# Kernel optimization log

Hardware: AMD Instinct MI355X
Metric: run time of the kernel (lower is better)

## Reference

```python
import jax, jax.numpy as jnp
import numpy as np

N = 1_000_000
D = 128            # node feature dim
G = 25_000         # number of graphs (num_segments, static)
STEPS = 8


def setup_inputs() -> dict:
    key = jax.random.key(0)
    k1, k2, k3 = jax.random.split(key, 3)
    node_feature = jax.random.normal(k1, (N, D), dtype=jnp.float32)
    graph_indicator = jnp.sort(jax.random.randint(k2, (N,), 0, G, dtype=jnp.int32))
    # glorot-ish small init for recurrent kernel (carry_dim=2D -> 4*D gates)
    recurrent_kernel = jax.random.normal(k3, (2 * D, 4 * D), dtype=jnp.float32) * 0.05
    bias = jnp.zeros((4 * D,), dtype=jnp.float32)
    return {
        "node_feature": node_feature,
        "graph_indicator": graph_indicator,
        "recurrent_kernel": recurrent_kernel,
        "bias": bias,
    }


def _segment_softmax(score, seg_ids, num_segments):
    # numerically-stable per-segment softmax over a flat score vector [N]
    smax = jax.ops.segment_max(score, seg_ids, num_segments=num_segments)
    e = jnp.exp(score - smax[seg_ids])
    denom = jax.ops.segment_sum(e, seg_ids, num_segments=num_segments)
    return e / denom[seg_ids]


def reference(node_feature, graph_indicator, recurrent_kernel, bias):
    d = node_feature.shape[-1]
    memory_state = jnp.zeros((G, d), dtype=node_feature.dtype)
    carry_state = jnp.zeros((G, d), dtype=node_feature.dtype)
    carry_state_evolved = None
    for _ in range(STEPS):
        # attention score per node: <node_feature, carry of its graph>
        carry_exp = carry_state[graph_indicator]                  # [N, d]
        score = jnp.sum(node_feature * carry_exp, axis=1)         # [N]
        attn = _segment_softmax(score, graph_indicator, G)        # [N]
        readout = jax.ops.segment_sum(attn[:, None] * node_feature,
                                      graph_indicator, num_segments=G)  # [G, d]
        carry_state_evolved = jnp.concatenate([carry_state, readout], axis=1)  # [G, 2d]
        # NoInputLSTMCell
        z = carry_state_evolved @ recurrent_kernel + bias          # [G, 4d]
        u, f, c, o = jnp.split(z, 4, axis=1)
        memory_state = jax.nn.sigmoid(f) * memory_state + jax.nn.sigmoid(u) * jnp.tanh(c)
        carry_state = jax.nn.sigmoid(o) * jnp.tanh(memory_state)
    return carry_state_evolved
```

## Files before the change

kernel.cpp:

```cpp
#include <hip/hip_runtime.h>
#include <stdint.h>

#define DD   128
#define G2D  256
#define G4D  512
#define GPB  8
#define SLOT 64
#define ASTR 264

typedef float  f32x4  __attribute__((ext_vector_type(4)));
typedef short  s16x4  __attribute__((ext_vector_type(4)));
typedef short  s16x8  __attribute__((ext_vector_type(8)));
typedef __bf16 bf16x8 __attribute__((ext_vector_type(8)));

__device__ __forceinline__ short f2bf(float f) {
  unsigned u = __builtin_bit_cast(unsigned, f);
  u += 0x7FFFu + ((u >> 16) & 1u);
  return (short)(u >> 16);
}
__device__ __forceinline__ float bf2f(short s) {
  unsigned u = ((unsigned)(unsigned short)s) << 16;
  return __builtin_bit_cast(float, u);
}
__device__ __forceinline__ float sigmoidf_(float x) {
  return 1.f / (1.f + __expf(-x));
}
__device__ __forceinline__ float tanhf_(float x) {
  x = fminf(fmaxf(x, -15.f), 15.f);
  float e = __expf(2.f * x);
  return (e - 1.f) / (e + 1.f);
}

__global__ void seg_kernel(const int* __restrict__ ind, int* __restrict__ seg,
                           int N, int G) {
  int g = blockIdx.x * blockDim.x + threadIdx.x;
  if (g > G) return;
  int lo = 0, hi = N;
  while (lo < hi) {
    int mid = (lo + hi) >> 1;
    if (ind[mid] < g) lo = mid + 1; else hi = mid;
  }
  seg[g] = lo;
}

__global__ void wconv_kernel(const float* __restrict__ W, short* __restrict__ WT) {
  int idx = blockIdx.x * blockDim.x + threadIdx.x;
  int n = idx & (G4D - 1);
  int k = idx >> 9;
  WT[(size_t)n * G2D + k] = f2bf(W[(size_t)k * G4D + n]);
}

__global__ void __launch_bounds__(512) fused_kernel(
    const float* __restrict__ nf, const int* __restrict__ seg,
    const short* __restrict__ WT, const float* __restrict__ bias,
    float* __restrict__ out, int G) {
  extern __shared__ char smem[];
  short* nfb   = (short*)smem;
  short* A     = (short*)(smem + GPB * SLOT * DD * 2);
  float* carry = (float*)(smem + GPB * SLOT * DD * 2 + 16 * ASTR * 2);
  float* mem   = (float*)((char*)carry + GPB * DD * 4);

  const int t    = threadIdx.x;
  const int w    = t >> 6;
  const int lane = t & 63;
  const int gq   = lane >> 4;
  const int sl   = lane & 15;
  const int g0   = blockIdx.x * GPB;
  const int g    = g0 + w;
  const bool active = (g < G);

  {
    int* az = (int*)A;
    for (int i = t; i < (16 * ASTR) / 2; i += 512) az[i] = 0;
    for (int i = t; i < GPB * DD; i += 512) mem[i] = 0.f;
  }
  int s0 = 0, n = 0;
  if (active) { s0 = seg[g]; n = seg[g + 1] - s0; }
  carry[w * DD + lane]      = 0.f;
  carry[w * DD + 64 + lane] = 0.f;
  __syncthreads();

  short* slot = nfb + w * (SLOT * DD);
  const int nl = n < SLOT ? n : SLOT;
  {
    const int r2 = lane >> 5;
    const int c  = lane & 31;
    const int iters = (nl + 1) >> 1;
    f32x4 vc; int rowc = r2; bool okc = rowc < nl;
    if (okc) vc = *((const f32x4*)(nf + (size_t)(s0 + rowc) * DD) + c);
    for (int i = 0; i < iters; ++i) {
      const int rown = (i + 1) * 2 + r2;
      f32x4 vn; const bool okn = rown < nl;
      if (okn) vn = *((const f32x4*)(nf + (size_t)(s0 + rown) * DD) + c);
      if (okc) {
        s16x4 o;
        o[0] = f2bf(vc.x); o[1] = f2bf(vc.y); o[2] = f2bf(vc.z); o[3] = f2bf(vc.w);
        *(s16x4*)(slot + (size_t)rowc * DD + c * 4) = o;
      }
      vc = vn; rowc = rown; okc = okn;
    }
  }

  s16x8 bw[8][4];
  #pragma unroll
  for (int kc = 0; kc < 8; ++kc) {
    const int k0 = kc * 32 + gq * 8;
    #pragma unroll
    for (int gi = 0; gi < 4; ++gi) {
      const int ncol = gi * DD + w * 16 + sl;
      bw[kc][gi] = *(const s16x8*)(WT + (size_t)ncol * G2D + k0);
    }
  }
  const int colB = w * 16 + sl;
  const float bU = bias[0 * DD + colB], bF = bias[1 * DD + colB],
              bC = bias[2 * DD + colB], bO = bias[3 * DD + colB];

  #pragma unroll 1
  for (int step = 0; step < 8; ++step) {
    float r[8];
    #pragma unroll
    for (int k = 0; k < 8; ++k) r[k] = 0.f;

    if (active && n > 0) {
      float m = -1e30f, l = 0.f;
      float acc[8];
      #pragma unroll
      for (int k = 0; k < 8; ++k) acc[k] = 0.f;

      if (step == 0) {
        const int nfull = nl >> 2, rem = nl & 3;
        #pragma unroll 2
        for (int i = 0; i < nfull; ++i) {
          s16x8 xr = *(const s16x8*)(slot + (size_t)(i * 4 + gq) * DD + sl * 8);
          #pragma unroll
          for (int k = 0; k < 8; ++k) acc[k] += bf2f(xr[k]);
          l += 1.f;
        }
        if (gq < rem) {
          s16x8 xr = *(const s16x8*)(slot + (size_t)(nfull * 4 + gq) * DD + sl * 8);
          #pragma unroll
          for (int k = 0; k < 8; ++k) acc[k] += bf2f(xr[k]);
          l += 1.f;
        }
        for (int j = SLOT + gq; j < n; j += 4) {
          const f32x4* gp = (const f32x4*)(nf + (size_t)(s0 + j) * DD) + sl * 2;
          const f32x4 a = gp[0], b = gp[1];
          const float xf[8] = {a.x, a.y, a.z, a.w, b.x, b.y, b.z, b.w};
          #pragma unroll
          for (int k = 0; k < 8; ++k) acc[k] += xf[k];
          l += 1.f;
        }
        m = 0.f;
      } else {
        const f32x4 c0 = *(const f32x4*)(carry + w * DD + sl * 8);
        const f32x4 c1 = *(const f32x4*)(carry + w * DD + sl * 8 + 4);
        auto upd = [&](const float xf[8]) {
          float s = xf[0] * c0.x + xf[1] * c0.y + xf[2] * c0.z + xf[3] * c0.w
                  + xf[4] * c1.x + xf[5] * c1.y + xf[6] * c1.z + xf[7] * c1.w;
          #pragma unroll
          for (int off = 1; off < 16; off <<= 1) s += __shfl_xor(s, off, 64);
          const float nm = fmaxf(m, s);
          const float sc = __expf(m - nm);
          const float p  = __expf(s - nm);
          l = l * sc + p;
          #pragma unroll
          for (int k = 0; k < 8; ++k) acc[k] = acc[k] * sc + p * xf[k];
          m = nm;
        };
        const int nfull = nl >> 2, rem = nl & 3;
        #pragma unroll 2
        for (int i = 0; i < nfull; ++i) {
          s16x8 xr = *(const s16x8*)(slot + (size_t)(i * 4 + gq) * DD + sl * 8);
          float xf[8];
          #pragma unroll
          for (int k = 0; k < 8; ++k) xf[k] = bf2f(xr[k]);
          upd(xf);
        }
        if (gq < rem) {
          s16x8 xr = *(const s16x8*)(slot + (size_t)(nfull * 4 + gq) * DD + sl * 8);
          float xf[8];
          #pragma unroll
          for (int k = 0; k < 8; ++k) xf[k] = bf2f(xr[k]);
          upd(xf);
        }
        for (int j = SLOT + gq; j < n; j += 4) {
          const f32x4* gp = (const f32x4*)(nf + (size_t)(s0 + j) * DD) + sl * 2;
          const f32x4 a = gp[0], b = gp[1];
          const float xf[8] = {a.x, a.y, a.z, a.w, b.x, b.y, b.z, b.w};
          upd(xf);
        }
      }
      #pragma unroll
      for (int ww = 16; ww <= 32; ww <<= 1) {
        const float m2 = __shfl_xor(m, ww, 64);
        const float l2 = __shfl_xor(l, ww, 64);
        const float M  = fmaxf(m, m2);
        const float e1 = __expf(m - M);
        const float e2 = __expf(m2 - M);
        l = l * e1 + l2 * e2;
        #pragma unroll
        for (int k = 0; k < 8; ++k) {
          const float a2 = __shfl_xor(acc[k], ww, 64);
          acc[k] = acc[k] * e1 + a2 * e2;
        }
        m = M;
      }
      if (gq == 0) {
        const float inv = (l > 0.f) ? 1.f / l : 0.f;
        s16x8 pk;
        #pragma unroll
        for (int k = 0; k < 8; ++k) { r[k] = acc[k] * inv; pk[k] = f2bf(r[k]); }
        *(s16x8*)(A + w * ASTR + DD + sl * 8) = pk;
      }
    }

    if (step == 7) {
      if (active) {
        if (gq == 0) {
          f32x4 r0 = {r[0], r[1], r[2], r[3]};
          f32x4 r1 = {r[4], r[5], r[6], r[7]};
          *(f32x4*)(out + (size_t)g * G2D + DD + sl * 8)     = r0;
          *(f32x4*)(out + (size_t)g * G2D + DD + sl * 8 + 4) = r1;
        } else if (gq == 1) {
          const f32x4 a = *(const f32x4*)(carry + w * DD + sl * 8);
          const f32x4 b = *(const f32x4*)(carry + w * DD + sl * 8 + 4);
          *(f32x4*)(out + (size_t)g * G2D + sl * 8)     = a;
          *(f32x4*)(out + (size_t)g * G2D + sl * 8 + 4) = b;
        }
      }
      break;
    }
    __syncthreads();

    f32x4 az[4];
    #pragma unroll
    for (int gi = 0; gi < 4; ++gi) az[gi] = (f32x4){0.f, 0.f, 0.f, 0.f};
    #pragma unroll
    for (int kc = 0; kc < 8; ++kc) {
      const int k0 = kc * 32 + gq * 8;
      const s16x8 af = *(const s16x8*)(A + (size_t)sl * ASTR + k0);
      #pragma unroll
      for (int gi = 0; gi < 4; ++gi)
        az[gi] = __builtin_amdgcn_mfma_f32_16x16x32_bf16(
            __builtin_bit_cast(bf16x8, af), __builtin_bit_cast(bf16x8, bw[kc][gi]),
            az[gi], 0, 0, 0);
    }
    __syncthreads();
    if (gq < 2) {
      #pragma unroll
      for (int rr = 0; rr < 4; ++rr) {
        const int gg = gq * 4 + rr;
        if (g0 + gg < G) {
          const float u = az[0][rr] + bU;
          const float f = az[1][rr] + bF;
          const float c = az[2][rr] + bC;
          const float o = az[3][rr] + bO;
          const float mo = mem[gg * DD + colB];
          const float mn = sigmoidf_(f) * mo + sigmoidf_(u) * tanhf_(c);
          mem[gg * DD + colB] = mn;
          const float cn = sigmoidf_(o) * tanhf_(mn);
          carry[gg * DD + colB] = cn;
          A[gg * ASTR + colB] = f2bf(cn);
        }
      }
    }
    __syncthreads();
  }
}

extern "C" void kernel_launch(void* const* d_in, const int* in_sizes, int n_in,
                              void* d_out, int out_size, void* d_ws, size_t ws_size,
                              hipStream_t stream) {
  const float* nf   = (const float*)d_in[0];
  const int*   ind  = (const int*)d_in[1];
  const float* W    = (const float*)d_in[2];
  const float* bias = (const float*)d_in[3];
  int N = in_sizes[1];
  int G = out_size / G2D;

  char* ws = (char*)d_ws;
  short* WT  = (short*)ws;
  int*   seg = (int*)(ws + 262144);
  (void)ws_size; (void)n_in;

  seg_kernel<<<(G + 256) / 256, 256, 0, stream>>>(ind, seg, N, G);
  wconv_kernel<<<(G2D * G4D) / 256, 256, 0, stream>>>(W, WT);

  const int SMEM_BYTES = GPB * SLOT * DD * 2
                       + 16 * ASTR * 2
                       + GPB * DD * 4
                       + GPB * DD * 4;
  static bool attr_set = false;
  if (!attr_set) {
    hipFuncSetAttribute(reinterpret_cast<const void*>(fused_kernel),
                        hipFuncAttributeMaxDynamicSharedMemorySize, SMEM_BYTES);
    attr_set = true;
  }
  fused_kernel<<<(G + GPB - 1) / GPB, 512, SMEM_BYTES, stream>>>(
      nf, seg, WT, bias, (float*)d_out, G);
}
```

Baseline: 1.319 ms.

## Split each graph across two waves with DPP reductions and lazy softmax rescaling

Doubles the block to 1024 threads so each graph is processed by two wavefronts, each taking half the nodes. The two partial online-softmax states are merged through a shared buffer, and the LSTM gate matmul is split so each wave computes two of the four gate groups. The shuffle-based 16-lane score reduction is replaced with DPP row adds, and the online softmax only rescales when the max grows by more than 8. This adds extra barriers and shared-memory traffic for the merges, and halves the registers available per thread.

Result: slower. 1.411 ms (+7.0%).

```diff
diff --git a/kernel.cpp b/kernel.cpp
--- a/kernel.cpp
+++ b/kernel.cpp
@@ -11,6 +11,7 @@
 typedef float  f32x4  __attribute__((ext_vector_type(4)));
 typedef short  s16x4  __attribute__((ext_vector_type(4)));
 typedef short  s16x8  __attribute__((ext_vector_type(8)));
+typedef int    i32x4  __attribute__((ext_vector_type(4)));
 typedef __bf16 bf16x8 __attribute__((ext_vector_type(8)));
 
 __device__ __forceinline__ short f2bf(float f) {
@@ -18,9 +19,9 @@
   u += 0x7FFFu + ((u >> 16) & 1u);
   return (short)(u >> 16);
 }
-__device__ __forceinline__ float bf2f(short s) {
-  unsigned u = ((unsigned)(unsigned short)s) << 16;
-  return __builtin_bit_cast(float, u);
+__device__ __forceinline__ void unpack2(int w_, float& lo, float& hi) {
+  lo = __builtin_bit_cast(float, (int)(w_ << 16));
+  hi = __builtin_bit_cast(float, (int)(w_ & 0xFFFF0000));
 }
 __device__ __forceinline__ float sigmoidf_(float x) {
   return 1.f / (1.f + __expf(-x));
@@ -29,6 +30,20 @@
   x = fminf(fmaxf(x, -15.f), 15.f);
   float e = __expf(2.f * x);
   return (e - 1.f) / (e + 1.f);
+}
+
+template <int CTRL>
+__device__ __forceinline__ float dppadd_(float v) {
+  const int x = __builtin_amdgcn_update_dpp(
+      0, __builtin_bit_cast(int, v), CTRL, 0xF, 0xF, true);
+  return v + __builtin_bit_cast(float, x);
+}
+__device__ __forceinline__ float reduce16(float v) {
+  v = dppadd_<0x128>(v);
+  v = dppadd_<0x124>(v);
+  v = dppadd_<0x122>(v);
+  v = dppadd_<0x121>(v);
+  return v;
 }
 
 __global__ void seg_kernel(const int* __restrict__ ind, int* __restrict__ seg,
@@ -50,7 +65,7 @@
   WT[(size_t)n * G2D + k] = f2bf(W[(size_t)k * G4D + n]);
 }
 
-__global__ void __launch_bounds__(512) fused_kernel(
+__global__ void __launch_bounds__(1024) fused_kernel(
     const float* __restrict__ nf, const int* __restrict__ seg,
     const short* __restrict__ WT, const float* __restrict__ bias,
     float* __restrict__ out, int G) {
@@ -58,38 +73,38 @@
   short* nfb   = (short*)smem;
   short* A     = (short*)(smem + GPB * SLOT * DD * 2);
   float* carry = (float*)(smem + GPB * SLOT * DD * 2 + 16 * ASTR * 2);
-  float* mem   = (float*)((char*)carry + GPB * DD * 4);
+  float* mem   = carry + GPB * DD;
+  float* xbuf  = mem + GPB * DD;
 
   const int t    = threadIdx.x;
   const int w    = t >> 6;
   const int lane = t & 63;
   const int gq   = lane >> 4;
   const int sl   = lane & 15;
+  const int gl   = w >> 1;
+  const int wp   = w & 1;
   const int g0   = blockIdx.x * GPB;
-  const int g    = g0 + w;
+  const int g    = g0 + gl;
   const bool active = (g < G);
 
   {
     int* az = (int*)A;
-    for (int i = t; i < (16 * ASTR) / 2; i += 512) az[i] = 0;
-    for (int i = t; i < GPB * DD; i += 512) mem[i] = 0.f;
+    for (int i = t; i < (16 * ASTR) / 2; i += 1024) az[i] = 0;
+    if (t < GPB * DD) { mem[t] = 0.f; carry[t] = 0.f; }
   }
   int s0 = 0, n = 0;
   if (active) { s0 = seg[g]; n = seg[g + 1] - s0; }
-  carry[w * DD + lane]      = 0.f;
-  carry[w * DD + 64 + lane] = 0.f;
-  __syncthreads();
-
-  short* slot = nfb + w * (SLOT * DD);
+
+  short* slot = nfb + gl * (SLOT * DD);
   const int nl = n < SLOT ? n : SLOT;
   {
-    const int r2 = lane >> 5;
+    const int r4 = (wp << 1) | (lane >> 5);
     const int c  = lane & 31;
-    const int iters = (nl + 1) >> 1;
-    f32x4 vc; int rowc = r2; bool okc = rowc < nl;
+    f32x4 vc; int rowc = r4; bool okc = rowc < nl;
     if (okc) vc = *((const f32x4*)(nf + (size_t)(s0 + rowc) * DD) + c);
+    const int iters = (nl + 3) >> 2;
     for (int i = 0; i < iters; ++i) {
-      const int rown = (i + 1) * 2 + r2;
+      const int rown = (i + 1) * 4 + r4;
       f32x4 vn; const bool okn = rown < nl;
       if (okn) vn = *((const f32x4*)(nf + (size_t)(s0 + rown) * DD) + c);
       if (okc) {
@@ -101,166 +116,170 @@
     }
   }
 
-  s16x8 bw[8][4];
+  s16x8 bw[8][2];
   #pragma unroll
-  for (int kc = 0; kc < 8; ++kc) {
-    const int k0 = kc * 32 + gq * 8;
+  for (int kc = 0; kc < 8; ++kc)
     #pragma unroll
-    for (int gi = 0; gi < 4; ++gi) {
-      const int ncol = gi * DD + w * 16 + sl;
-      bw[kc][gi] = *(const s16x8*)(WT + (size_t)ncol * G2D + k0);
-    }
-  }
-  const int colB = w * 16 + sl;
-  const float bU = bias[0 * DD + colB], bF = bias[1 * DD + colB],
+    for (int j = 0; j < 2; ++j) {
+      const int ncol = (wp * 2 + j) * DD + gl * 16 + sl;
+      bw[kc][j] = *(const s16x8*)(WT + (size_t)ncol * G2D + kc * 32 + gq * 8);
+    }
+  const int colB = gl * 16 + sl;
+  const float bU = bias[colB],          bF = bias[DD + colB],
               bC = bias[2 * DD + colB], bO = bias[3 * DD + colB];
+
+  __syncthreads();
 
   #pragma unroll 1
   for (int step = 0; step < 8; ++step) {
-    float r[8];
+    const bool noscore = (step == 0);
+    const f32x4 c0 = *(const f32x4*)(carry + gl * DD + sl * 8);
+    const f32x4 c1 = *(const f32x4*)(carry + gl * DD + sl * 8 + 4);
+
+    float m = -1e30f, l = 0.f, acc[8];
     #pragma unroll
-    for (int k = 0; k < 8; ++k) r[k] = 0.f;
+    for (int k = 0; k < 8; ++k) acc[k] = 0.f;
+    const int off = wp * 4 + gq;
+
+    auto score = [&](const float xf[8]) -> float {
+      float a = fmaf(xf[1], c0.y, xf[0] * c0.x);
+      float b = fmaf(xf[3], c0.w, xf[2] * c0.z);
+      float c = fmaf(xf[5], c1.y, xf[4] * c1.x);
+      float d = fmaf(xf[7], c1.w, xf[6] * c1.z);
+      return reduce16((a + b) + (c + d));
+    };
+    auto upd = [&](const float xf[8], float s) {
+      if (s > m + 8.f) {
+        const float sc = __expf(m - s);
+        l *= sc;
+        #pragma unroll
+        for (int k = 0; k < 8; ++k) acc[k] *= sc;
+        m = s;
+      }
+      const float p = __expf(s - m);
+      l += p;
+      #pragma unroll
+      for (int k = 0; k < 8; ++k) acc[k] = fmaf(p, xf[k], acc[k]);
+    };
 
     if (active && n > 0) {
-      float m = -1e30f, l = 0.f;
-      float acc[8];
-      #pragma unroll
-      for (int k = 0; k < 8; ++k) acc[k] = 0.f;
-
-      if (step == 0) {
-        const int nfull = nl >> 2, rem = nl & 3;
-        #pragma unroll 2
-        for (int i = 0; i < nfull; ++i) {
-          s16x8 xr = *(const s16x8*)(slot + (size_t)(i * 4 + gq) * DD + sl * 8);
-          #pragma unroll
-          for (int k = 0; k < 8; ++k) acc[k] += bf2f(xr[k]);
-          l += 1.f;
-        }
-        if (gq < rem) {
-          s16x8 xr = *(const s16x8*)(slot + (size_t)(nfull * 4 + gq) * DD + sl * 8);
-          #pragma unroll
-          for (int k = 0; k < 8; ++k) acc[k] += bf2f(xr[k]);
-          l += 1.f;
-        }
-        for (int j = SLOT + gq; j < n; j += 4) {
-          const f32x4* gp = (const f32x4*)(nf + (size_t)(s0 + j) * DD) + sl * 2;
-          const f32x4 a = gp[0], b = gp[1];
-          const float xf[8] = {a.x, a.y, a.z, a.w, b.x, b.y, b.z, b.w};
-          #pragma unroll
-          for (int k = 0; k < 8; ++k) acc[k] += xf[k];
-          l += 1.f;
-        }
-        m = 0.f;
-      } else {
-        const f32x4 c0 = *(const f32x4*)(carry + w * DD + sl * 8);
-        const f32x4 c1 = *(const f32x4*)(carry + w * DD + sl * 8 + 4);
-        auto upd = [&](const float xf[8]) {
-          float s = xf[0] * c0.x + xf[1] * c0.y + xf[2] * c0.z + xf[3] * c0.w
-                  + xf[4] * c1.x + xf[5] * c1.y + xf[6] * c1.z + xf[7] * c1.w;
-          #pragma unroll
-          for (int off = 1; off < 16; off <<= 1) s += __shfl_xor(s, off, 64);
-          const float nm = fmaxf(m, s);
-          const float sc = __expf(m - nm);
-          const float p  = __expf(s - nm);
-          l = l * sc + p;
-          #pragma unroll
-          for (int k = 0; k < 8; ++k) acc[k] = acc[k] * sc + p * xf[k];
-          m = nm;
-        };
-        const int nfull = nl >> 2, rem = nl & 3;
-        #pragma unroll 2
-        for (int i = 0; i < nfull; ++i) {
-          s16x8 xr = *(const s16x8*)(slot + (size_t)(i * 4 + gq) * DD + sl * 8);
-          float xf[8];
-          #pragma unroll
-          for (int k = 0; k < 8; ++k) xf[k] = bf2f(xr[k]);
-          upd(xf);
-        }
-        if (gq < rem) {
-          s16x8 xr = *(const s16x8*)(slot + (size_t)(nfull * 4 + gq) * DD + sl * 8);
-          float xf[8];
-          #pragma unroll
-          for (int k = 0; k < 8; ++k) xf[k] = bf2f(xr[k]);
-          upd(xf);
-        }
-        for (int j = SLOT + gq; j < n; j += 4) {
-          const f32x4* gp = (const f32x4*)(nf + (size_t)(s0 + j) * DD) + sl * 2;
-          const f32x4 a = gp[0], b = gp[1];
-          const float xf[8] = {a.x, a.y, a.z, a.w, b.x, b.y, b.z, b.w};
-          upd(xf);
-        }
+      const short* bp = slot + (size_t)off * DD + sl * 8;
+      const int nfull = nl >> 3;
+      i32x4 xr;
+      if (nfull > 0) xr = *(const i32x4*)bp;
+      for (int i = 0; i < nfull; ++i) {
+        i32x4 xn = *(const i32x4*)(bp + (size_t)(i + 1) * 8 * DD);
+        float xf[8];
+        unpack2(xr.x, xf[0], xf[1]); unpack2(xr.y, xf[2], xf[3]);
+        unpack2(xr.z, xf[4], xf[5]); unpack2(xr.w, xf[6], xf[7]);
+        const float s = noscore ? 0.f : score(xf);
+        upd(xf, s);
+        xr = xn;
+      }
+      const int rem = nl & 7;
+      if (off < rem) {
+        const i32x4 xv = *(const i32x4*)(bp + (size_t)nfull * 8 * DD);
+        float xf[8];
+        unpack2(xv.x, xf[0], xf[1]); unpack2(xv.y, xf[2], xf[3]);
+        unpack2(xv.z, xf[4], xf[5]); unpack2(xv.w, xf[6], xf[7]);
+        const float s = noscore ? 0.f : score(xf);
+        upd(xf, s);
+      }
+      for (int j = SLOT + off; j < n; j += 8) {
+        const f32x4* gp = (const f32x4*)(nf + (size_t)(s0 + j) * DD) + sl * 2;
+        const f32x4 a = gp[0], b = gp[1];
+        const float xf[8] = {a.x, a.y, a.z, a.w, b.x, b.y, b.z, b.w};
+        const float s = noscore ? 0.f : score(xf);
+        upd(xf, s);
       }
       #pragma unroll
       for (int ww = 16; ww <= 32; ww <<= 1) {
         const float m2 = __shfl_xor(m, ww, 64);
         const float l2 = __shfl_xor(l, ww, 64);
         const float M  = fmaxf(m, m2);
-        const float e1 = __expf(m - M);
-        const float e2 = __expf(m2 - M);
+        const float e1 = __expf(m - M), e2 = __expf(m2 - M);
         l = l * e1 + l2 * e2;
         #pragma unroll
-        for (int k = 0; k < 8; ++k) {
-          const float a2 = __shfl_xor(acc[k], ww, 64);
-          acc[k] = acc[k] * e1 + a2 * e2;
-        }
+        for (int k = 0; k < 8; ++k)
+          acc[k] = acc[k] * e1 + __shfl_xor(acc[k], ww, 64) * e2;
         m = M;
       }
-      if (gq == 0) {
-        const float inv = (l > 0.f) ? 1.f / l : 0.f;
-        s16x8 pk;
-        #pragma unroll
-        for (int k = 0; k < 8; ++k) { r[k] = acc[k] * inv; pk[k] = f2bf(r[k]); }
-        *(s16x8*)(A + w * ASTR + DD + sl * 8) = pk;
-      }
-    }
-
+    }
+
+    float* xb = xbuf + (gl * 16 + sl) * 12;
+    if (wp == 1 && gq == 0) {
+      *(f32x4*)(xb)     = (f32x4){acc[0], acc[1], acc[2], acc[3]};
+      *(f32x4*)(xb + 4) = (f32x4){acc[4], acc[5], acc[6], acc[7]};
+      xb[8] = m; xb[9] = l;
+    }
+    __syncthreads();
+    if (wp == 0 && gq == 0) {
+      const float m2 = xb[8], l2 = xb[9];
+      const f32x4 a0 = *(const f32x4*)xb, a1 = *(const f32x4*)(xb + 4);
+      const float a2[8] = {a0.x, a0.y, a0.z, a0.w, a1.x, a1.y, a1.z, a1.w};
+      const float M  = fmaxf(m, m2);
+      const float e1 = __expf(m - M), e2 = __expf(m2 - M);
+      const float L  = l * e1 + l2 * e2;
+      const float inv = (L > 0.f) ? 1.f / L : 0.f;
+      float r[8];
+      s16x8 pk;
+      #pragma unroll
+      for (int k = 0; k < 8; ++k) {
+        r[k]  = (acc[k] * e1 + a2[k] * e2) * inv;
+        pk[k] = f2bf(r[k]);
+      }
+      *(s16x8*)(A + gl * ASTR + DD + sl * 8) = pk;
+      if (step == 7 && active) {
+        *(f32x4*)(out + (size_t)g * G2D + DD + sl * 8)     = (f32x4){r[0], r[1], r[2], r[3]};
+        *(f32x4*)(out + (size_t)g * G2D + DD + sl * 8 + 4) = (f32x4){r[4], r[5], r[6], r[7]};
+      }
+    }
     if (step == 7) {
-      if (active) {
-        if (gq == 0) {
-          f32x4 r0 = {r[0], r[1], r[2], r[3]};
-          f32x4 r1 = {r[4], r[5], r[6], r[7]};
-          *(f32x4*)(out + (size_t)g * G2D + DD + sl * 8)     = r0;
-          *(f32x4*)(out + (size_t)g * G2D + DD + sl * 8 + 4) = r1;
-        } else if (gq == 1) {
-          const f32x4 a = *(const f32x4*)(carry + w * DD + sl * 8);
-          const f32x4 b = *(const f32x4*)(carry + w * DD + sl * 8 + 4);
-          *(f32x4*)(out + (size_t)g * G2D + sl * 8)     = a;
-          *(f32x4*)(out + (size_t)g * G2D + sl * 8 + 4) = b;
-        }
+      if (wp == 0 && gq == 1 && active) {
+        *(f32x4*)(out + (size_t)g * G2D + sl * 8) =
+            *(const f32x4*)(carry + gl * DD + sl * 8);
+        *(f32x4*)(out + (size_t)g * G2D + sl * 8 + 4) =
+            *(const f32x4*)(carry + gl * DD + sl * 8 + 4);
       }
       break;
     }
     __syncthreads();
 
-    f32x4 az[4];
-    #pragma unroll
-    for (int gi = 0; gi < 4; ++gi) az[gi] = (f32x4){0.f, 0.f, 0.f, 0.f};
+    f32x4 az[2] = {(f32x4){0.f, 0.f, 0.f, 0.f}, (f32x4){0.f, 0.f, 0.f, 0.f}};
     #pragma unroll
     for (int kc = 0; kc < 8; ++kc) {
-      const int k0 = kc * 32 + gq * 8;
-      const s16x8 af = *(const s16x8*)(A + (size_t)sl * ASTR + k0);
-      #pragma unroll
-      for (int gi = 0; gi < 4; ++gi)
-        az[gi] = __builtin_amdgcn_mfma_f32_16x16x32_bf16(
-            __builtin_bit_cast(bf16x8, af), __builtin_bit_cast(bf16x8, bw[kc][gi]),
-            az[gi], 0, 0, 0);
+      const s16x8 af = *(const s16x8*)(A + (size_t)sl * ASTR + kc * 32 + gq * 8);
+      #pragma unroll
+      for (int j = 0; j < 2; ++j)
+        az[j] = __builtin_amdgcn_mfma_f32_16x16x32_bf16(
+            __builtin_bit_cast(bf16x8, af), __builtin_bit_cast(bf16x8, bw[kc][j]),
+            az[j], 0, 0, 0);
+    }
+    if (wp == 1 && gq < 2) {
+      #pragma unroll
+      for (int j = 0; j < 2; ++j)
+        #pragma unroll
+        for (int rr = 0; rr < 4; ++rr) {
+          const int row = gq * 4 + rr;
+          xbuf[((gl * 2 + j) * 8 + row) * 16 + sl] = az[j][rr];
+        }
     }
     __syncthreads();
-    if (gq < 2) {
+    if (wp == 0 && gq < 2) {
       #pragma unroll
       for (int rr = 0; rr < 4; ++rr) {
-        const int gg = gq * 4 + rr;
-        if (g0 + gg < G) {
-          const float u = az[0][rr] + bU;
-          const float f = az[1][rr] + bF;
-          const float c = az[2][rr] + bC;
-          const float o = az[3][rr] + bO;
-          const float mo = mem[gg * DD + colB];
+        const int row = gq * 4 + rr;
+        if (g0 + row < G) {
+          const float u  = az[0][rr] + bU;
+          const float f  = az[1][rr] + bF;
+          const float c  = xbuf[((gl * 2 + 0) * 8 + row) * 16 + sl] + bC;
+          const float o  = xbuf[((gl * 2 + 1) * 8 + row) * 16 + sl] + bO;
+          const float mo = mem[row * DD + colB];
           const float mn = sigmoidf_(f) * mo + sigmoidf_(u) * tanhf_(c);
-          mem[gg * DD + colB] = mn;
+          mem[row * DD + colB] = mn;
           const float cn = sigmoidf_(o) * tanhf_(mn);
-          carry[gg * DD + colB] = cn;
-          A[gg * ASTR + colB] = f2bf(cn);
+          carry[row * DD + colB] = cn;
+          A[row * ASTR + colB] = f2bf(cn);
         }
       }
     }
@@ -289,13 +308,14 @@
   const int SMEM_BYTES = GPB * SLOT * DD * 2
                        + 16 * ASTR * 2
                        + GPB * DD * 4
-                       + GPB * DD * 4;
+                       + GPB * DD * 4
+                       + 8192;
   static bool attr_set = false;
   if (!attr_set) {
     hipFuncSetAttribute(reinterpret_cast<const void*>(fused_kernel),
                         hipFuncAttributeMaxDynamicSharedMemorySize, SMEM_BYTES);
     attr_set = true;
   }
-  fused_kernel<<<(G + GPB - 1) / GPB, 512, SMEM_BYTES, stream>>>(
+  fused_kernel<<<(G + GPB - 1) / GPB, 1024, SMEM_BYTES, stream>>>(
       nf, seg, WT, bias, (float*)d_out, G);
 }
```
